# Performance work log

Measured on AMD Instinct MI355X. Metric: run time of the kernel, lower is better.

## Reference

```python
import jax, jax.numpy as jnp
import numpy as np

B, S, HID, H = 8, 128, 256, 4
DH = HID // H
FF = 4 * HID


def setup_inputs() -> dict:
    key = jax.random.key(0)
    ks = jax.random.split(key, 16)
    n = lambda i, shape: jax.random.normal(ks[i], shape, dtype=jnp.float32) * 0.02
    z = lambda shape: jnp.zeros(shape, dtype=jnp.float32)
    return dict(
        x=jax.random.normal(ks[0], (B, S, HID), dtype=jnp.float32),
        attention_mask=jnp.zeros((B, 1, S, S), dtype=jnp.float32),
        Wq=n(1, (HID, HID)), bq=z((HID,)),
        Wk=n(2, (HID, HID)), bk=z((HID,)),
        Wv=n(3, (HID, HID)), bv=z((HID,)),
        order_w=n(4, (2 * DH,)), order_b=z(()),
        dist_w=n(5, (2 * DH,)), dist_b=z(()),
        scalar=jax.random.normal(ks[6], (1,), dtype=jnp.float32),
        AWq=n(7, (HID, HID)), Abq=z((HID,)),
        AWk=n(8, (HID, HID)), Abk=z((HID,)),
        Wd=n(9, (HID, HID)), bd=z((HID,)),
        g1=jnp.ones((HID,), jnp.float32), beta1=z((HID,)),
        W1=n(10, (HID, FF)), b1=z((FF,)),
        W2=n(11, (FF, HID)), b2=z((HID,)),
        g2=jnp.ones((HID,), jnp.float32), beta2=z((HID,)),
    )


def _ln(t, g, b, eps=1e-12):
    m = t.mean(-1, keepdims=True)
    v = ((t - m) ** 2).mean(-1, keepdims=True)
    return (t - m) / jnp.sqrt(v + eps) * g + b


def _heads(t):
    # [B,S,HID] -> [B,H,S,DH]
    return t.reshape(B, S, H, DH).transpose(0, 2, 1, 3)


def reference(x, attention_mask, Wq, bq, Wk, bk, Wv, bv, order_w, order_b,
              dist_w, dist_b, scalar, AWq, Abq, AWk, Abk, Wd, bd,
              g1, beta1, W1, b1, W2, b2, g2, beta2):
    inv = 1.0 / jnp.sqrt(jnp.float32(DH))
    q = x @ Wq + bq
    k = x @ Wk + bk
    v = x @ Wv + bv
    qh, kh, vh = _heads(q), _heads(k), _heads(v)
    scores = jnp.einsum('bhqd,bhkd->bhqk', qh, kh)  # [B,H,S,S]

    # order/distance affines on concat(q_i, k_j): Linear(2*DH,1) decomposes into
    # per-token projections summed via broadcast (same math, no [B,H,S,S,2*DH] tensor)
    pr_order = jax.nn.sigmoid((qh @ order_w[:DH])[..., :, None]
                              + (kh @ order_w[DH:])[..., None, :] + order_b)
    gd_order = jnp.triu(jnp.ones((S, S), jnp.float32), k=1)
    err_order = (jnp.log(pr_order + 1e-24) * gd_order
                 + jnp.log(1.0 - pr_order + 1e-24) * (1.0 - gd_order))

    idx = jnp.arange(S)
    gd_dist = jnp.log(jnp.abs(idx[None, :] - idx[:, None]).astype(jnp.float32) + 1.0)
    pr_dist = ((qh @ dist_w[:DH])[..., :, None]
               + (kh @ dist_w[DH:])[..., None, :] + dist_b)
    err_dist = -jnp.square(gd_dist - pr_dist) * jnp.square(scalar[0]) * 0.5

    rich_scores = scores + err_order + err_dist
    softm = lambda s: jax.nn.softmax(s * inv + attention_mask, axis=-1)
    rich_probs = softm(rich_scores)
    origin_probs = softm(scores)

    # rich/calibrated combine ('fixed'): softmax(origin + 0.5 * rich)
    combined = jax.nn.softmax(origin_probs + 0.5 * rich_probs, axis=-1)

    # two-level attack attention on transformed mixed q/k
    aq, ak = _heads(q @ AWq + Abq), _heads(k @ AWk + Abk)
    attack_probs = softm(jnp.einsum('bhqd,bhkd->bhqk', aq, ak))
    final_probs = jax.nn.softmax(combined + 0.5 * attack_probs, axis=-1)

    ctx = jnp.einsum('bhqk,bhkd->bhqd', final_probs, vh)
    ctx = ctx.transpose(0, 2, 1, 3).reshape(B, S, HID)
    h = _ln(ctx @ Wd + bd + x, g1, beta1)
    f = jax.nn.gelu(h @ W1 + b1, approximate=False) @ W2 + b2
    return _ln(f + h, g2, beta2)
```

## Files before the change

### kernel.cpp

```cpp
#include <hip/hip_runtime.h>
#include <hip/hip_bf16.h>
#include <math.h>

#define B_  8
#define S_  128
#define HID_ 256
#define H_  4
#define DH_ 64
#define FF_ 1024
#define M_  (B_ * S_)

typedef _Float16 half_t;
typedef __attribute__((ext_vector_type(8))) _Float16 half8;
typedef __attribute__((ext_vector_type(4))) float floatx4;

enum { EP_F32 = 0, EP_F16 = 1, EP_F16B = 2, EP_GELU = 3, EP_PROJ = 4 };

__device__ __forceinline__ floatx4 mfma16(half8 a, half8 b, floatx4 c) {
    return __builtin_amdgcn_mfma_f32_16x16x32_f16(a, b, c, 0, 0, 0);
}

__device__ __forceinline__ float wred_sum(float v) {
#pragma unroll
    for (int o = 32; o >= 1; o >>= 1) v += __shfl_xor(v, o, 64);
    return v;
}
__device__ __forceinline__ float wred_max(float v) {
#pragma unroll
    for (int o = 32; o >= 1; o >>= 1) v = fmaxf(v, __shfl_xor(v, o, 64));
    return v;
}
__device__ __forceinline__ float block_sum_256(float v, float* s4, int tid) {
    v = wred_sum(v);
    __syncthreads();
    if ((tid & 63) == 0) s4[tid >> 6] = v;
    __syncthreads();
    return s4[0] + s4[1] + s4[2] + s4[3];
}
__device__ __forceinline__ float2 softmax2(float2 l) {
    float m = wred_max(fmaxf(l.x, l.y));
    float e0 = expf(l.x - m), e1 = expf(l.y - m);
    float s = wred_sum(e0 + e1);
    float r = 1.f / s;
    return make_float2(e0 * r, e1 * r);
}

template<int EPI>
__device__ __forceinline__ void mgemm(
    const half_t* __restrict__ A, int ldA,
    const half_t* __restrict__ Bt, int ldB,
    int kLen, int m0, int n0,
    const float* __restrict__ bias,
    float* __restrict__ Cf, half_t* __restrict__ Ch, int ldC,
    const float* __restrict__ pw1, const float* __restrict__ pw2,
    float* __restrict__ po1, float* __restrict__ po2, int hsel)
{
    __shared__ half8 Asf[2][4][64];
    __shared__ half8 Bsf[2][4][64];

    const int tid = threadIdx.x;
    const int w = tid >> 6, l = tid & 63;
    const int sr = tid >> 2;
    const int sq = tid & 3;
    const int sdst = (sr & 15) | (sq << 4);
    const int smt = sr >> 4;
    const half_t* Ap = A + (size_t)(m0 + sr) * ldA + sq * 8;
    const half_t* Bp = Bt + (size_t)(n0 + sr) * ldB + sq * 8;

    half8 ra, rb;
    auto fetch = [&](int t) {
        ra = *(const half8*)(Ap + t * 32);
        rb = *(const half8*)(Bp + t * 32);
    };
    auto commit = [&](int buf) {
        Asf[buf][smt][sdst] = ra;
        Bsf[buf][smt][sdst] = rb;
    };

    floatx4 zero = {0.f, 0.f, 0.f, 0.f};
    floatx4 acc[4] = {zero, zero, zero, zero};
    const int kt = kLen >> 5;

    fetch(0);
    commit(0);
    __syncthreads();
    for (int t = 0; t < kt; ++t) {
        const bool more = (t + 1 < kt);
        if (more) fetch(t + 1);
        const int buf = t & 1;
        half8 a = Asf[buf][w][l];
        acc[0] = mfma16(a, Bsf[buf][0][l], acc[0]);
        acc[1] = mfma16(a, Bsf[buf][1][l], acc[1]);
        acc[2] = mfma16(a, Bsf[buf][2][l], acc[2]);
        acc[3] = mfma16(a, Bsf[buf][3][l], acc[3]);
        __syncthreads();
        if (more) {
            commit((t + 1) & 1);
            __syncthreads();
        }
    }

    const int quad = l >> 4, lc = l & 15;
    const int rowb = m0 + w * 16 + quad * 4;
    float bvv[4] = {0.f, 0.f, 0.f, 0.f};
    if (EPI >= EP_F16B) {
#pragma unroll
        for (int nt = 0; nt < 4; ++nt) bvv[nt] = bias[n0 + nt * 16 + lc];
    }
    float pw1v[4], pw2v[4];
    if (EPI == EP_PROJ) {
#pragma unroll
        for (int nt = 0; nt < 4; ++nt) {
            pw1v[nt] = pw1[nt * 16 + lc];
            pw2v[nt] = pw2[nt * 16 + lc];
        }
    }
#pragma unroll
    for (int rr = 0; rr < 4; ++rr) {
        float ov[4];
#pragma unroll
        for (int nt = 0; nt < 4; ++nt) {
            float o = acc[nt][rr];
            if (EPI >= EP_F16B) o += bvv[nt];
            if (EPI == EP_GELU) o = 0.5f * o * (1.f + erff(o * 0.70710678118654752f));
            ov[nt] = o;
            const size_t ci = (size_t)(rowb + rr) * ldC + n0 + nt * 16 + lc;
            if (EPI == EP_F32) Cf[ci] = o;
            else Ch[ci] = (half_t)o;
        }
        if (EPI == EP_PROJ) {
            float po = ov[0] * pw1v[0] + ov[1] * pw1v[1] + ov[2] * pw1v[2] + ov[3] * pw1v[3];
            float pd = ov[0] * pw2v[0] + ov[1] * pw2v[1] + ov[2] * pw2v[2] + ov[3] * pw2v[3];
#pragma unroll
            for (int off = 1; off < 16; off <<= 1) {
                po += __shfl_xor(po, off, 64);
                pd += __shfl_xor(pd, off, 64);
            }
            if (lc == 0) {
                const int m = rowb + rr;
                const int idx = ((m >> 7) * H_ + hsel) * S_ + (m & 127);
                po1[idx] = po;
                po2[idx] = pd;
            }
        }
    }
}

__global__ __launch_bounds__(256) void prep_kernel(
    const float* __restrict__ x,
    const float* __restrict__ Wq, const float* __restrict__ Wk,
    const float* __restrict__ Wv, const float* __restrict__ Wd,
    const float* __restrict__ AWq, const float* __restrict__ AWk,
    const float* __restrict__ W1, const float* __restrict__ W2,
    half_t* __restrict__ x16, half_t* __restrict__ Wq16n, half_t* __restrict__ Wk16n,
    half_t* __restrict__ WqT, half_t* __restrict__ WkT, half_t* __restrict__ WvT,
    half_t* __restrict__ WdT, half_t* __restrict__ AWqT, half_t* __restrict__ AWkT,
    half_t* __restrict__ W1T, half_t* __restrict__ W2T)
{
    const int z = blockIdx.z, bx = blockIdx.x, by = blockIdx.y;
    const int tid = threadIdx.x;
    if (z < 3) {
        const float* src = (z == 0) ? x : (z == 1) ? Wq : Wk;
        half_t* dst = (z == 0) ? x16 : (z == 1) ? Wq16n : Wk16n;
        const int total = (z == 0) ? M_ * HID_ : HID_ * HID_;
        const int bid = by * 16 + bx;
        if (bid * 1024 < total) {
            const int base = bid * 1024 + tid * 4;
            float4 vv = *(const float4*)(src + base);
            dst[base + 0] = (half_t)vv.x;
            dst[base + 1] = (half_t)vv.y;
            dst[base + 2] = (half_t)vv.z;
            dst[base + 3] = (half_t)vv.w;
        }
        return;
    }
    const float* src; half_t* dst; int K, N, k0, n0;
    if (z <= 8) {
        const float* ins[6] = {Wq, Wk, Wv, Wd, AWq, AWk};
        half_t* outs[6] = {WqT, WkT, WvT, WdT, AWqT, AWkT};
        src = ins[z - 3]; dst = outs[z - 3];
        K = 256; N = 256; k0 = bx * 64; n0 = by * 64;
        if (bx >= 4 || by >= 4) return;
    } else if (z == 9) {
        src = W1; dst = W1T; K = 256; N = 1024;
        k0 = bx * 64; n0 = by * 64;
        if (bx >= 4) return;
    } else {
        src = W2; dst = W2T; K = 1024; N = 256;
        k0 = by * 64; n0 = bx * 64;
        if (bx >= 4) return;
    }
    __shared__ half_t tl[64][72];
    const int r = tid >> 2, c0 = (tid & 3) * 16;
#pragma unroll 4
    for (int i = 0; i < 16; ++i)
        tl[c0 + i][r] = (half_t)src[(size_t)(k0 + r) * N + n0 + c0 + i];
    __syncthreads();
#pragma unroll 4
    for (int i = 0; i < 16; ++i)
        dst[(size_t)(n0 + r) * K + k0 + c0 + i] = tl[r][c0 + i];
}

__global__ __launch_bounds__(256) void compose_mfma(
    const half_t* __restrict__ AWqT, const half_t* __restrict__ AWkT,
    const half_t* __restrict__ Wq16n, const half_t* __restrict__ Wk16n,
    const float* __restrict__ AWq, const float* __restrict__ AWk,
    const float* __restrict__ bq, const float* __restrict__ bk,
    const float* __restrict__ Abq, const float* __restrict__ Abk,
    half_t* __restrict__ WcqT, half_t* __restrict__ WckT,
    float* __restrict__ bcq, float* __restrict__ bck)
{
    const int z = blockIdx.z;
    if (blockIdx.y < 4) {
        const half_t* A = z ? AWkT : AWqT;
        const half_t* Bt = z ? Wk16n : Wq16n;
        half_t* C = z ? WckT : WcqT;
        mgemm<EP_F16>(A, HID_, Bt, HID_, HID_, blockIdx.y * 64, blockIdx.x * 64,
                      nullptr, nullptr, C, HID_, nullptr, nullptr, nullptr, nullptr, 0);
    } else {
        __shared__ float red[4][64];
        const float* bsrc = z ? bk : bq;
        const float* AW   = z ? AWk : AWq;
        const float* Ab   = z ? Abk : Abq;
        float* bco        = z ? bck : bcq;
        int t = threadIdx.x, l = t & 63, kc = t >> 6;
        int n = blockIdx.x * 64 + l;
        float p = 0.f;
#pragma unroll 8
        for (int kk = 0; kk < 64; ++kk) {
            int k = kc * 64 + kk;
            p = fmaf(bsrc[k], AW[(size_t)k * HID_ + n], p);
        }
        red[kc][l] = p;
        __syncthreads();
        if (kc == 0)
            bco[n] = red[0][l] + red[1][l] + red[2][l] + red[3][l] + Ab[n];
    }
}

__global__ __launch_bounds__(256) void xgemm5(
    const half_t* __restrict__ x16,
    const half_t* __restrict__ WqT, const float* __restrict__ bq,
    const half_t* __restrict__ WkT, const float* __restrict__ bk,
    const half_t* __restrict__ WvT, const float* __restrict__ bv,
    const half_t* __restrict__ WcqT, const float* __restrict__ bcq,
    const half_t* __restrict__ WckT, const float* __restrict__ bck,
    const float* __restrict__ order_w, const float* __restrict__ dist_w,
    half_t* __restrict__ q16, half_t* __restrict__ k16, half_t* __restrict__ v16,
    half_t* __restrict__ aq16, half_t* __restrict__ ak16,
    float* __restrict__ qoA, float* __restrict__ qdA,
    float* __restrict__ koA, float* __restrict__ kdA)
{
    const int z = blockIdx.z;
    const int m0 = blockIdx.y * 64, n0 = blockIdx.x * 64;
    if (z == 0)
        mgemm<EP_PROJ>(x16, HID_, WqT, HID_, HID_, m0, n0, bq, nullptr, q16, HID_,
                       order_w, dist_w, qoA, qdA, blockIdx.x);
    else if (z == 1)
        mgemm<EP_PROJ>(x16, HID_, WkT, HID_, HID_, m0, n0, bk, nullptr, k16, HID_,
                       order_w + DH_, dist_w + DH_, koA, kdA, blockIdx.x);
    else if (z == 2)
        mgemm<EP_F16B>(x16, HID_, WvT, HID_, HID_, m0, n0, bv, nullptr, v16, HID_,
                       nullptr, nullptr, nullptr, nullptr, 0);
    else if (z == 3)
        mgemm<EP_F16B>(x16, HID_, WcqT, HID_, HID_, m0, n0, bcq, nullptr, aq16, HID_,
                       nullptr, nullptr, nullptr, nullptr, 0);
    else
        mgemm<EP_F16B>(x16, HID_, WckT, HID_, HID_, m0, n0, bck, nullptr, ak16, HID_,
                       nullptr, nullptr, nullptr, nullptr, 0);
}

__global__ __launch_bounds__(256) void score_mfma(
    const half_t* __restrict__ q16, const half_t* __restrict__ k16,
    const half_t* __restrict__ aq16, const half_t* __restrict__ ak16,
    float* __restrict__ scb, float* __restrict__ asb)
{
    const int type = blockIdx.z >> 5;
    const int bh = blockIdx.z & 31;
    const int b = bh >> 2, h = bh & 3;
    const size_t off = (size_t)b * S_ * HID_ + h * DH_;
    const half_t* A  = (type ? aq16 : q16) + off;
    const half_t* Bt = (type ? ak16 : k16) + off;
    float* C = (type ? asb : scb) + (size_t)bh * S_ * S_;
    mgemm<EP_F32>(A, HID_, Bt, HID_, DH_, blockIdx.y * 64, blockIdx.x * 64,
                  nullptr, C, nullptr, S_, nullptr, nullptr, nullptr, nullptr, 0);
}

__global__ __launch_bounds__(256) void softmax_pv(
    const float* __restrict__ scb, const float* __restrict__ asb,
    const half_t* __restrict__ v16,
    const float* __restrict__ qoA, const float* __restrict__ qdA,
    const float* __restrict__ koA, const float* __restrict__ kdA,
    const float* __restrict__ mask,
    const float* __restrict__ order_b_p, const float* __restrict__ dist_b_p,
    const float* __restrict__ scalar_p,
    half_t* __restrict__ ctx16)
{
    const int tid = threadIdx.x;
    const int wv = tid >> 6, lane = tid & 63;
    const int bh = blockIdx.x >> 5;
    const int quad = blockIdx.x & 31;
    const int i = quad * 4 + wv;
    const int b = bh >> 2, h = bh & 3;

    const size_t rowoff = ((size_t)bh * S_ + i) * S_ + 2 * lane;
    float2 sc2 = *(const float2*)&scb[rowoff];
    float2 at2 = *(const float2*)&asb[rowoff];
    float2 mk  = *(const float2*)&mask[((size_t)(b * S_ + i)) * S_ + 2 * lane];
    float2 ko  = *(const float2*)&koA[bh * S_ + 2 * lane];
    float2 kd  = *(const float2*)&kdA[bh * S_ + 2 * lane];
    float qo = qoA[bh * S_ + i];
    float qd = qdA[bh * S_ + i];
    float ob = order_b_p[0], db = dist_b_p[0];
    float scl = scalar_p[0];
    float s2 = scl * scl;
    const float inv = 0.125f;

    float2 rich;
    {
        int j = 2 * lane;
        float pr = 1.f / (1.f + expf(-(qo + ko.x + ob)));
        float sel = (j > i) ? pr : 1.f - pr;
        float erro = logf(sel + 1e-24f);
        float gd = logf(fabsf((float)(j - i)) + 1.f);
        float dd = gd - (qd + kd.x + db);
        rich.x = sc2.x + erro - 0.5f * dd * dd * s2;
    }
    {
        int j = 2 * lane + 1;
        float pr = 1.f / (1.f + expf(-(qo + ko.y + ob)));
        float sel = (j > i) ? pr : 1.f - pr;
        float erro = logf(sel + 1e-24f);
        float gd = logf(fabsf((float)(j - i)) + 1.f);
        float dd = gd - (qd + kd.y + db);
        rich.y = sc2.y + erro - 0.5f * dd * dd * s2;
    }

    float2 p0 = softmax2(make_float2(sc2.x * inv + mk.x, sc2.y * inv + mk.y));
    float2 p1 = softmax2(make_float2(rich.x * inv + mk.x, rich.y * inv + mk.y));
    float2 pc = softmax2(make_float2(p0.x + 0.5f * p1.x, p0.y + 0.5f * p1.y));
    float2 pa = softmax2(make_float2(at2.x * inv + mk.x, at2.y * inv + mk.y));
    float2 pf = softmax2(make_float2(pc.x + 0.5f * pa.x, pc.y + 0.5f * pa.y));

    const half_t* vb = v16 + (size_t)b * S_ * HID_ + h * DH_ + lane;
    float acc = 0.f;
#pragma unroll 8
    for (int jj = 0; jj < 64; ++jj) {
        float fx = __shfl(pf.x, jj, 64);
        float fy = __shfl(pf.y, jj, 64);
        acc = fmaf(fx, (float)vb[(size_t)(2 * jj) * HID_], acc);
        acc = fmaf(fy, (float)vb[(size_t)(2 * jj + 1) * HID_], acc);
    }
    ctx16[((size_t)(b * S_ + i)) * HID_ + h * DH_ + lane] = (half_t)acc;
}

__global__ __launch_bounds__(256) void dense_mfma(
    const half_t* __restrict__ ctx16, const half_t* __restrict__ WdT,
    float* __restrict__ dn)
{
    mgemm<EP_F32>(ctx16, HID_, WdT, HID_, HID_, blockIdx.y * 64, blockIdx.x * 64,
                  nullptr, dn, nullptr, HID_, nullptr, nullptr, nullptr, nullptr, 0);
}

__global__ __launch_bounds__(256) void ff1_mfma(
    const half_t* __restrict__ h16, const half_t* __restrict__ W1T,
    const float* __restrict__ b1, half_t* __restrict__ f116)
{
    mgemm<EP_GELU>(h16, HID_, W1T, HID_, HID_, blockIdx.y * 64, blockIdx.x * 64,
                   b1, nullptr, f116, FF_, nullptr, nullptr, nullptr, nullptr, 0);
}

__global__ __launch_bounds__(256) void ff2_mfma(
    const half_t* __restrict__ f116, const half_t* __restrict__ W2T,
    float* __restrict__ p0, float* __restrict__ p1)
{
    const int z = blockIdx.z;
    float* C = z ? p1 : p0;
    mgemm<EP_F32>(f116 + z * 512, FF_, W2T + z * 512, FF_, 512,
                  blockIdx.y * 64, blockIdx.x * 64,
                  nullptr, C, nullptr, HID_, nullptr, nullptr, nullptr, nullptr, 0);
}

__global__ __launch_bounds__(256) void ln1_kernel(
    const float* __restrict__ dn, const float* __restrict__ bd,
    const float* __restrict__ x,
    const float* __restrict__ g1, const float* __restrict__ beta1,
    float* __restrict__ h32, half_t* __restrict__ h16)
{
    __shared__ float s4[4];
    const int row = blockIdx.x;
    const int n = threadIdx.x;
    const size_t idx = (size_t)row * HID_ + n;
    float val = dn[idx] + bd[n] + x[idx];
    float mean = block_sum_256(val, s4, n) * (1.f / HID_);
    float dv = val - mean;
    float var = block_sum_256(dv * dv, s4, n) * (1.f / HID_);
    float r = dv * rsqrtf(var + 1e-12f) * g1[n] + beta1[n];
    h32[idx] = r;
    h16[idx] = (half_t)r;
}

__global__ __launch_bounds__(256) void ln2_kernel(
    const float* __restrict__ p0, const float* __restrict__ p1,
    const float* __restrict__ b2, const float* __restrict__ h32,
    const float* __restrict__ g2, const float* __restrict__ beta2,
    float* __restrict__ out)
{
    __shared__ float s4[4];
    const int row = blockIdx.x;
    const int n = threadIdx.x;
    const size_t idx = (size_t)row * HID_ + n;
    float val = p0[idx] + p1[idx] + b2[n] + h32[idx];
    float mean = block_sum_256(val, s4, n) * (1.f / HID_);
    float dv = val - mean;
    float var = block_sum_256(dv * dv, s4, n) * (1.f / HID_);
    out[idx] = dv * rsqrtf(var + 1e-12f) * g2[n] + beta2[n];
}

extern "C" void kernel_launch(void* const* d_in, const int* in_sizes, int n_in,
                              void* d_out, int out_size, void* d_ws, size_t ws_size,
                              hipStream_t stream) {
    const float* x        = (const float*)d_in[0];
    const float* mask     = (const float*)d_in[1];
    const float* Wq       = (const float*)d_in[2];
    const float* bq       = (const float*)d_in[3];
    const float* Wk       = (const float*)d_in[4];
    const float* bk       = (const float*)d_in[5];
    const float* Wv       = (const float*)d_in[6];
    const float* bv       = (const float*)d_in[7];
    const float* order_w  = (const float*)d_in[8];
    const float* order_b  = (const float*)d_in[9];
    const float* dist_w   = (const float*)d_in[10];
    const float* dist_b   = (const float*)d_in[11];
    const float* scalar   = (const float*)d_in[12];
    const float* AWq      = (const float*)d_in[13];
    const float* Abq      = (const float*)d_in[14];
    const float* AWk      = (const float*)d_in[15];
    const float* Abk      = (const float*)d_in[16];
    const float* Wd       = (const float*)d_in[17];
    const float* bd       = (const float*)d_in[18];
    const float* g1       = (const float*)d_in[19];
    const float* beta1    = (const float*)d_in[20];
    const float* W1       = (const float*)d_in[21];
    const float* b1       = (const float*)d_in[22];
    const float* W2       = (const float*)d_in[23];
    const float* b2       = (const float*)d_in[24];
    const float* g2       = (const float*)d_in[25];
    const float* beta2    = (const float*)d_in[26];

    float* ws = (float*)d_ws;
    size_t off = 0;
    auto afl = [&](size_t n) { float* p = ws + off; off += n; return p; };
    auto ahf = [&](size_t nhalves) { half_t* p = (half_t*)(ws + off); off += nhalves / 2; return p; };

    half_t* x16   = ahf(M_ * HID_);
    half_t* Wq16n = ahf(HID_ * HID_);
    half_t* Wk16n = ahf(HID_ * HID_);
    half_t* WqT   = ahf(HID_ * HID_);
    half_t* WkT   = ahf(HID_ * HID_);
    half_t* WvT   = ahf(HID_ * HID_);
    half_t* WdT   = ahf(HID_ * HID_);
    half_t* AWqT  = ahf(HID_ * HID_);
    half_t* AWkT  = ahf(HID_ * HID_);
    half_t* W1T   = ahf(HID_ * FF_);
    half_t* W2T   = ahf(HID_ * FF_);
    half_t* WcqT  = ahf(HID_ * HID_);
    half_t* WckT  = ahf(HID_ * HID_);
    half_t* q16   = ahf(M_ * HID_);
    half_t* k16   = ahf(M_ * HID_);
    half_t* v16   = ahf(M_ * HID_);
    half_t* aq16  = ahf(M_ * HID_);
    half_t* ak16  = ahf(M_ * HID_);
    half_t* ctx16 = ahf(M_ * HID_);
    half_t* h16   = ahf(M_ * HID_);
    half_t* f116  = ahf(M_ * FF_);
    float* scb  = afl((size_t)B_ * H_ * S_ * S_);
    float* asb  = afl((size_t)B_ * H_ * S_ * S_);
    float* dnb  = afl(M_ * HID_);
    float* hb32 = afl(M_ * HID_);
    float* pf0  = afl(M_ * HID_);
    float* pf1  = afl(M_ * HID_);
    float* bcq  = afl(256);
    float* bck  = afl(256);
    float* qoA  = afl(B_ * H_ * S_);
    float* qdA  = afl(B_ * H_ * S_);
    float* koA  = afl(B_ * H_ * S_);
    float* kdA  = afl(B_ * H_ * S_);

    prep_kernel<<<dim3(16, 16, 11), 256, 0, stream>>>(
        x, Wq, Wk, Wv, Wd, AWq, AWk, W1, W2,
        x16, Wq16n, Wk16n, WqT, WkT, WvT, WdT, AWqT, AWkT, W1T, W2T);
    compose_mfma<<<dim3(4, 5, 2), 256, 0, stream>>>(
        AWqT, AWkT, Wq16n, Wk16n, AWq, AWk, bq, bk, Abq, Abk, WcqT, WckT, bcq, bck);
    xgemm5<<<dim3(4, 16, 5), 256, 0, stream>>>(
        x16, WqT, bq, WkT, bk, WvT, bv, WcqT, bcq, WckT, bck, order_w, dist_w,
        q16, k16, v16, aq16, ak16, qoA, qdA, koA, kdA);
    score_mfma<<<dim3(2, 2, 64), 256, 0, stream>>>(q16, k16, aq16, ak16, scb, asb);
    softmax_pv<<<1024, 256, 0, stream>>>(scb, asb, v16, qoA, qdA, koA, kdA,
                                         mask, order_b, dist_b, scalar, ctx16);
    dense_mfma<<<dim3(4, 16), 256, 0, stream>>>(ctx16, WdT, dnb);
    ln1_kernel<<<M_, 256, 0, stream>>>(dnb, bd, x, g1, beta1, hb32, h16);
    ff1_mfma<<<dim3(16, 16), 256, 0, stream>>>(h16, W1T, b1, f116);
    ff2_mfma<<<dim3(4, 16, 2), 256, 0, stream>>>(f116, W2T, pf0, pf1);
    ln2_kernel<<<M_, 256, 0, stream>>>(pf0, pf1, b2, hb32, g2, beta2, (float*)d_out);
}
```

Baseline: 171.8 us.

## Fuse score GEMMs, softmax chain and PV into one attention kernel; fuse GEMM+LayerNorm

Replaces the separate score GEMM and softmax/PV kernels with a single attention kernel per (batch, head, query-half) that computes both score matrices with MFMA, runs the five-softmax chain in registers, and does PV with MFMA through shared memory. The dense and FF2 GEMMs are each fused with their following LayerNorm into a full-row kernel, and the split-K FF2 partial buffers go away. This removes the fp32 score round trips through global memory and several launches, but it also cuts parallelism to 64 and 16 blocks, which may underfill the GPU.

Result: slower. 199.2 us (+15.9%).

```diff
diff --git a/kernel.cpp b/kernel.cpp
--- a/kernel.cpp
+++ b/kernel.cpp
@@ -11,6 +11,7 @@
 #define M_  (B_ * S_)
 
 typedef _Float16 half_t;
+typedef __attribute__((ext_vector_type(4))) _Float16 half4;
 typedef __attribute__((ext_vector_type(8))) _Float16 half8;
 typedef __attribute__((ext_vector_type(4))) float floatx4;
 
@@ -20,29 +21,28 @@
     return __builtin_amdgcn_mfma_f32_16x16x32_f16(a, b, c, 0, 0, 0);
 }
 
-__device__ __forceinline__ float wred_sum(float v) {
-#pragma unroll
-    for (int o = 32; o >= 1; o >>= 1) v += __shfl_xor(v, o, 64);
+__device__ __forceinline__ float qred_sum(float v) {
+#pragma unroll
+    for (int o = 1; o < 16; o <<= 1) v += __shfl_xor(v, o, 64);
     return v;
 }
-__device__ __forceinline__ float wred_max(float v) {
-#pragma unroll
-    for (int o = 32; o >= 1; o >>= 1) v = fmaxf(v, __shfl_xor(v, o, 64));
+__device__ __forceinline__ float qred_max(float v) {
+#pragma unroll
+    for (int o = 1; o < 16; o <<= 1) v = fmaxf(v, __shfl_xor(v, o, 64));
     return v;
 }
-__device__ __forceinline__ float block_sum_256(float v, float* s4, int tid) {
-    v = wred_sum(v);
-    __syncthreads();
-    if ((tid & 63) == 0) s4[tid >> 6] = v;
-    __syncthreads();
-    return s4[0] + s4[1] + s4[2] + s4[3];
-}
-__device__ __forceinline__ float2 softmax2(float2 l) {
-    float m = wred_max(fmaxf(l.x, l.y));
-    float e0 = expf(l.x - m), e1 = expf(l.y - m);
-    float s = wred_sum(e0 + e1);
+__device__ __forceinline__ void sm8(float (&v)[8]) {
+    float m = v[0];
+#pragma unroll
+    for (int j = 1; j < 8; ++j) m = fmaxf(m, v[j]);
+    m = qred_max(m);
+    float s = 0.f;
+#pragma unroll
+    for (int j = 0; j < 8; ++j) { v[j] = expf(v[j] - m); s += v[j]; }
+    s = qred_sum(s);
     float r = 1.f / s;
-    return make_float2(e0 * r, e1 * r);
+#pragma unroll
+    for (int j = 0; j < 8; ++j) v[j] *= r;
 }
 
 template<int EPI>
@@ -270,25 +270,10 @@
                        nullptr, nullptr, nullptr, nullptr, 0);
 }
 
-__global__ __launch_bounds__(256) void score_mfma(
+__global__ __launch_bounds__(256) void attn_fused(
     const half_t* __restrict__ q16, const half_t* __restrict__ k16,
-    const half_t* __restrict__ aq16, const half_t* __restrict__ ak16,
-    float* __restrict__ scb, float* __restrict__ asb)
-{
-    const int type = blockIdx.z >> 5;
-    const int bh = blockIdx.z & 31;
-    const int b = bh >> 2, h = bh & 3;
-    const size_t off = (size_t)b * S_ * HID_ + h * DH_;
-    const half_t* A  = (type ? aq16 : q16) + off;
-    const half_t* Bt = (type ? ak16 : k16) + off;
-    float* C = (type ? asb : scb) + (size_t)bh * S_ * S_;
-    mgemm<EP_F32>(A, HID_, Bt, HID_, DH_, blockIdx.y * 64, blockIdx.x * 64,
-                  nullptr, C, nullptr, S_, nullptr, nullptr, nullptr, nullptr, 0);
-}
-
-__global__ __launch_bounds__(256) void softmax_pv(
-    const float* __restrict__ scb, const float* __restrict__ asb,
-    const half_t* __restrict__ v16,
+    const half_t* __restrict__ v16, const half_t* __restrict__ aq16,
+    const half_t* __restrict__ ak16,
     const float* __restrict__ qoA, const float* __restrict__ qdA,
     const float* __restrict__ koA, const float* __restrict__ kdA,
     const float* __restrict__ mask,
@@ -296,70 +281,235 @@
     const float* __restrict__ scalar_p,
     half_t* __restrict__ ctx16)
 {
+    __shared__ half8 Qf[2][4][64], AQf[2][4][64];
+    __shared__ half8 Kf[2][8][64], AKf[2][8][64];
+    __shared__ half_t Vs[128][68];
+    __shared__ half_t Pm[64][136];
+
     const int tid = threadIdx.x;
-    const int wv = tid >> 6, lane = tid & 63;
-    const int bh = blockIdx.x >> 5;
-    const int quad = blockIdx.x & 31;
-    const int i = quad * 4 + wv;
+    const int w = tid >> 6, l = tid & 63;
+    const int quad = l >> 4, lc = l & 15;
+    const int bid = blockIdx.x;
+    const int bh = bid >> 1, it = bid & 1;
     const int b = bh >> 2, h = bh & 3;
-
-    const size_t rowoff = ((size_t)bh * S_ + i) * S_ + 2 * lane;
-    float2 sc2 = *(const float2*)&scb[rowoff];
-    float2 at2 = *(const float2*)&asb[rowoff];
-    float2 mk  = *(const float2*)&mask[((size_t)(b * S_ + i)) * S_ + 2 * lane];
-    float2 ko  = *(const float2*)&koA[bh * S_ + 2 * lane];
-    float2 kd  = *(const float2*)&kdA[bh * S_ + 2 * lane];
-    float qo = qoA[bh * S_ + i];
-    float qd = qdA[bh * S_ + i];
-    float ob = order_b_p[0], db = dist_b_p[0];
-    float scl = scalar_p[0];
-    float s2 = scl * scl;
+    const size_t hoff = (size_t)b * S_ * HID_ + h * DH_;
+
+#pragma unroll
+    for (int u = 0; u < 2; ++u) {
+        int idx = tid * 2 + u;
+        int r = idx >> 3, c = idx & 7;
+        const size_t g = hoff + (size_t)(it * 64 + r) * HID_ + c * 8;
+        int kt = c >> 2, mt = r >> 4, sl = (r & 15) | ((c & 3) << 4);
+        Qf[kt][mt][sl]  = *(const half8*)(q16 + g);
+        AQf[kt][mt][sl] = *(const half8*)(aq16 + g);
+    }
+#pragma unroll
+    for (int u = 0; u < 4; ++u) {
+        int idx = tid * 4 + u;
+        int j = idx >> 3, c = idx & 7;
+        const size_t g = hoff + (size_t)j * HID_ + c * 8;
+        int kt = c >> 2, jt = j >> 4, sl = (j & 15) | ((c & 3) << 4);
+        Kf[kt][jt][sl]  = *(const half8*)(k16 + g);
+        AKf[kt][jt][sl] = *(const half8*)(ak16 + g);
+        half8 vv = *(const half8*)(v16 + g);
+        half4 v0 = {vv[0], vv[1], vv[2], vv[3]};
+        half4 v1 = {vv[4], vv[5], vv[6], vv[7]};
+        *(half4*)&Vs[j][c * 8]     = v0;
+        *(half4*)&Vs[j][c * 8 + 4] = v1;
+    }
+    __syncthreads();
+
+    floatx4 zero = {0.f, 0.f, 0.f, 0.f};
+    floatx4 accS[8], accA[8];
+#pragma unroll
+    for (int jt = 0; jt < 8; ++jt) { accS[jt] = zero; accA[jt] = zero; }
+#pragma unroll
+    for (int kt = 0; kt < 2; ++kt) {
+        half8 a0 = Qf[kt][w][l];
+        half8 a1 = AQf[kt][w][l];
+#pragma unroll
+        for (int jt = 0; jt < 8; ++jt) {
+            accS[jt] = mfma16(a0, Kf[kt][jt][l], accS[jt]);
+            accA[jt] = mfma16(a1, AKf[kt][jt][l], accA[jt]);
+        }
+    }
+
+    const float ob = order_b_p[0], db = dist_b_p[0];
+    const float scl = scalar_p[0];
+    const float s2 = scl * scl;
     const float inv = 0.125f;
-
-    float2 rich;
-    {
-        int j = 2 * lane;
-        float pr = 1.f / (1.f + expf(-(qo + ko.x + ob)));
-        float sel = (j > i) ? pr : 1.f - pr;
-        float erro = logf(sel + 1e-24f);
-        float gd = logf(fabsf((float)(j - i)) + 1.f);
-        float dd = gd - (qd + kd.x + db);
-        rich.x = sc2.x + erro - 0.5f * dd * dd * s2;
-    }
-    {
-        int j = 2 * lane + 1;
-        float pr = 1.f / (1.f + expf(-(qo + ko.y + ob)));
-        float sel = (j > i) ? pr : 1.f - pr;
-        float erro = logf(sel + 1e-24f);
-        float gd = logf(fabsf((float)(j - i)) + 1.f);
-        float dd = gd - (qd + kd.y + db);
-        rich.y = sc2.y + erro - 0.5f * dd * dd * s2;
-    }
-
-    float2 p0 = softmax2(make_float2(sc2.x * inv + mk.x, sc2.y * inv + mk.y));
-    float2 p1 = softmax2(make_float2(rich.x * inv + mk.x, rich.y * inv + mk.y));
-    float2 pc = softmax2(make_float2(p0.x + 0.5f * p1.x, p0.y + 0.5f * p1.y));
-    float2 pa = softmax2(make_float2(at2.x * inv + mk.x, at2.y * inv + mk.y));
-    float2 pf = softmax2(make_float2(pc.x + 0.5f * pa.x, pc.y + 0.5f * pa.y));
-
-    const half_t* vb = v16 + (size_t)b * S_ * HID_ + h * DH_ + lane;
-    float acc = 0.f;
-#pragma unroll 8
-    for (int jj = 0; jj < 64; ++jj) {
-        float fx = __shfl(pf.x, jj, 64);
-        float fy = __shfl(pf.y, jj, 64);
-        acc = fmaf(fx, (float)vb[(size_t)(2 * jj) * HID_], acc);
-        acc = fmaf(fy, (float)vb[(size_t)(2 * jj + 1) * HID_], acc);
-    }
-    ctx16[((size_t)(b * S_ + i)) * HID_ + h * DH_ + lane] = (half_t)acc;
-}
-
-__global__ __launch_bounds__(256) void dense_mfma(
-    const half_t* __restrict__ ctx16, const half_t* __restrict__ WdT,
-    float* __restrict__ dn)
+    float kov[8], kdv[8];
+#pragma unroll
+    for (int jt = 0; jt < 8; ++jt) {
+        kov[jt] = koA[bh * S_ + jt * 16 + lc];
+        kdv[jt] = kdA[bh * S_ + jt * 16 + lc];
+    }
+    const int il_base = w * 16 + quad * 4;
+#pragma unroll
+    for (int reg = 0; reg < 4; ++reg) {
+        const int il = il_base + reg;
+        const int i  = it * 64 + il;
+        float qo = qoA[bh * S_ + i], qd = qdA[bh * S_ + i];
+        const float* mrow = mask + ((size_t)(b * S_ + i)) * S_;
+        float mk[8], lg[8], as_[8];
+#pragma unroll
+        for (int jt = 0; jt < 8; ++jt) {
+            mk[jt] = mrow[jt * 16 + lc];
+            lg[jt] = accS[jt][reg];
+            as_[jt] = accA[jt][reg];
+        }
+        float p0[8];
+#pragma unroll
+        for (int jt = 0; jt < 8; ++jt) p0[jt] = lg[jt] * inv + mk[jt];
+        sm8(p0);
+        float p1[8];
+#pragma unroll
+        for (int jt = 0; jt < 8; ++jt) {
+            int j = jt * 16 + lc;
+            float pr = 1.f / (1.f + expf(-(qo + kov[jt] + ob)));
+            float sel = (j > i) ? pr : 1.f - pr;
+            float erro = logf(sel + 1e-24f);
+            float gd = logf(fabsf((float)(j - i)) + 1.f);
+            float dd = gd - (qd + kdv[jt] + db);
+            p1[jt] = (lg[jt] + erro - 0.5f * dd * dd * s2) * inv + mk[jt];
+        }
+        sm8(p1);
+#pragma unroll
+        for (int jt = 0; jt < 8; ++jt) p0[jt] += 0.5f * p1[jt];
+        sm8(p0);
+#pragma unroll
+        for (int jt = 0; jt < 8; ++jt) p1[jt] = as_[jt] * inv + mk[jt];
+        sm8(p1);
+#pragma unroll
+        for (int jt = 0; jt < 8; ++jt) p0[jt] += 0.5f * p1[jt];
+        sm8(p0);
+#pragma unroll
+        for (int jt = 0; jt < 8; ++jt) Pm[il][jt * 16 + lc] = (half_t)p0[jt];
+    }
+    __syncthreads();
+
+    half8 pa_[4];
+#pragma unroll
+    for (int kt = 0; kt < 4; ++kt)
+        pa_[kt] = *(const half8*)&Pm[w * 16 + lc][kt * 32 + quad * 8];
+    floatx4 apv[4];
+#pragma unroll
+    for (int nt = 0; nt < 4; ++nt) apv[nt] = zero;
+#pragma unroll
+    for (int nt = 0; nt < 4; ++nt) {
+#pragma unroll
+        for (int kt = 0; kt < 4; ++kt) {
+            half8 vf;
+#pragma unroll
+            for (int e = 0; e < 8; ++e)
+                vf[e] = Vs[kt * 32 + quad * 8 + e][nt * 16 + lc];
+            apv[nt] = mfma16(pa_[kt], vf, apv[nt]);
+        }
+    }
+#pragma unroll
+    for (int nt = 0; nt < 4; ++nt) {
+#pragma unroll
+        for (int reg = 0; reg < 4; ++reg) {
+            int i = it * 64 + w * 16 + quad * 4 + reg;
+            ctx16[hoff + (size_t)i * HID_ + nt * 16 + lc] = (half_t)apv[nt][reg];
+        }
+    }
+}
+
+template<int WRITE16>
+__global__ __launch_bounds__(256) void gemmln(
+    const half_t* __restrict__ A, const half_t* __restrict__ Bt, int K,
+    const float* __restrict__ bias, const float* __restrict__ res,
+    const float* __restrict__ g, const float* __restrict__ be,
+    float* __restrict__ out32, half_t* __restrict__ out16)
 {
-    mgemm<EP_F32>(ctx16, HID_, WdT, HID_, HID_, blockIdx.y * 64, blockIdx.x * 64,
-                  nullptr, dn, nullptr, HID_, nullptr, nullptr, nullptr, nullptr, 0);
+    __shared__ half8 Asf[2][4][64];
+    __shared__ half8 Bsf[2][16][64];
+
+    const int tid = threadIdx.x;
+    const int w = tid >> 6, l = tid & 63;
+    const int quad = l >> 4, lc = l & 15;
+    const int m0 = blockIdx.x * 64;
+
+    const int ar = tid >> 2, aq_ = tid & 3;
+    const half_t* Ap = A + (size_t)(m0 + ar) * K + aq_ * 8;
+    const half_t* Bp = Bt + (size_t)tid * K;
+
+    half8 ra, rb[4];
+    auto fetch = [&](int t) {
+        ra = *(const half8*)(Ap + t * 32);
+        const half_t* bp = Bp + t * 32;
+#pragma unroll
+        for (int u = 0; u < 4; ++u) rb[u] = *(const half8*)(bp + u * 8);
+    };
+    auto commit = [&](int buf) {
+        Asf[buf][ar >> 4][(ar & 15) | (aq_ << 4)] = ra;
+#pragma unroll
+        for (int u = 0; u < 4; ++u)
+            Bsf[buf][tid >> 4][(tid & 15) | (u << 4)] = rb[u];
+    };
+
+    floatx4 zero = {0.f, 0.f, 0.f, 0.f};
+    floatx4 acc[16];
+#pragma unroll
+    for (int nt = 0; nt < 16; ++nt) acc[nt] = zero;
+    const int kt = K >> 5;
+
+    fetch(0);
+    commit(0);
+    __syncthreads();
+    for (int t = 0; t < kt; ++t) {
+        const bool more = (t + 1 < kt);
+        if (more) fetch(t + 1);
+        const int buf = t & 1;
+        half8 a = Asf[buf][w][l];
+#pragma unroll
+        for (int nt = 0; nt < 16; ++nt)
+            acc[nt] = mfma16(a, Bsf[buf][nt][l], acc[nt]);
+        __syncthreads();
+        if (more) {
+            commit((t + 1) & 1);
+            __syncthreads();
+        }
+    }
+
+    float bv[16], gg[16], bb[16];
+#pragma unroll
+    for (int nt = 0; nt < 16; ++nt) {
+        bv[nt] = bias[nt * 16 + lc];
+        gg[nt] = g[nt * 16 + lc];
+        bb[nt] = be[nt * 16 + lc];
+    }
+#pragma unroll
+    for (int reg = 0; reg < 4; ++reg) {
+        const int row = m0 + w * 16 + quad * 4 + reg;
+        const float* rr = res + (size_t)row * HID_;
+        float vals[16];
+        float s = 0.f;
+#pragma unroll
+        for (int nt = 0; nt < 16; ++nt) {
+            vals[nt] = acc[nt][reg] + bv[nt] + rr[nt * 16 + lc];
+            s += vals[nt];
+        }
+        s = qred_sum(s);
+        float mean = s * (1.f / HID_);
+        float vs = 0.f;
+#pragma unroll
+        for (int nt = 0; nt < 16; ++nt) {
+            float d = vals[nt] - mean;
+            vals[nt] = d;
+            vs += d * d;
+        }
+        vs = qred_sum(vs);
+        float rstd = rsqrtf(vs * (1.f / HID_) + 1e-12f);
+#pragma unroll
+        for (int nt = 0; nt < 16; ++nt) {
+            float o = vals[nt] * rstd * gg[nt] + bb[nt];
+            const size_t ci = (size_t)row * HID_ + nt * 16 + lc;
+            out32[ci] = o;
+            if (WRITE16) out16[ci] = (half_t)o;
+        }
+    }
 }
 
 __global__ __launch_bounds__(256) void ff1_mfma(
@@ -368,53 +518,6 @@
 {
     mgemm<EP_GELU>(h16, HID_, W1T, HID_, HID_, blockIdx.y * 64, blockIdx.x * 64,
                    b1, nullptr, f116, FF_, nullptr, nullptr, nullptr, nullptr, 0);
-}
-
-__global__ __launch_bounds__(256) void ff2_mfma(
-    const half_t* __restrict__ f116, const half_t* __restrict__ W2T,
-    float* __restrict__ p0, float* __restrict__ p1)
-{
-    const int z = blockIdx.z;
-    float* C = z ? p1 : p0;
-    mgemm<EP_F32>(f116 + z * 512, FF_, W2T + z * 512, FF_, 512,
-                  blockIdx.y * 64, blockIdx.x * 64,
-                  nullptr, C, nullptr, HID_, nullptr, nullptr, nullptr, nullptr, 0);
-}
-
-__global__ __launch_bounds__(256) void ln1_kernel(
-    const float* __restrict__ dn, const float* __restrict__ bd,
-    const float* __restrict__ x,
-    const float* __restrict__ g1, const float* __restrict__ beta1,
-    float* __restrict__ h32, half_t* __restrict__ h16)
-{
-    __shared__ float s4[4];
-    const int row = blockIdx.x;
-    const int n = threadIdx.x;
-    const size_t idx = (size_t)row * HID_ + n;
-    float val = dn[idx] + bd[n] + x[idx];
-    float mean = block_sum_256(val, s4, n) * (1.f / HID_);
-    float dv = val - mean;
-    float var = block_sum_256(dv * dv, s4, n) * (1.f / HID_);
-    float r = dv * rsqrtf(var + 1e-12f) * g1[n] + beta1[n];
-    h32[idx] = r;
-    h16[idx] = (half_t)r;
-}
-
-__global__ __launch_bounds__(256) void ln2_kernel(
-    const float* __restrict__ p0, const float* __restrict__ p1,
-    const float* __restrict__ b2, const float* __restrict__ h32,
-    const float* __restrict__ g2, const float* __restrict__ beta2,
-    float* __restrict__ out)
-{
-    __shared__ float s4[4];
-    const int row = blockIdx.x;
-    const int n = threadIdx.x;
-    const size_t idx = (size_t)row * HID_ + n;
-    float val = p0[idx] + p1[idx] + b2[n] + h32[idx];
-    float mean = block_sum_256(val, s4, n) * (1.f / HID_);
-    float dv = val - mean;
-    float var = block_sum_256(dv * dv, s4, n) * (1.f / HID_);
-    out[idx] = dv * rsqrtf(var + 1e-12f) * g2[n] + beta2[n];
 }
 
 extern "C" void kernel_launch(void* const* d_in, const int* in_sizes, int n_in,
@@ -451,7 +554,7 @@
     float* ws = (float*)d_ws;
     size_t off = 0;
     auto afl = [&](size_t n) { float* p = ws + off; off += n; return p; };
-    auto ahf = [&](size_t nhalves) { half_t* p = (half_t*)(ws + off); off += nhalves / 2; return p; };
+    auto ahf = [&](size_t nh) { half_t* p = (half_t*)(ws + off); off += nh / 2; return p; };
 
     half_t* x16   = ahf(M_ * HID_);
     half_t* Wq16n = ahf(HID_ * HID_);
@@ -474,12 +577,7 @@
     half_t* ctx16 = ahf(M_ * HID_);
     half_t* h16   = ahf(M_ * HID_);
     half_t* f116  = ahf(M_ * FF_);
-    float* scb  = afl((size_t)B_ * H_ * S_ * S_);
-    float* asb  = afl((size_t)B_ * H_ * S_ * S_);
-    float* dnb  = afl(M_ * HID_);
     float* hb32 = afl(M_ * HID_);
-    float* pf0  = afl(M_ * HID_);
-    float* pf1  = afl(M_ * HID_);
     float* bcq  = afl(256);
     float* bck  = afl(256);
     float* qoA  = afl(B_ * H_ * S_);
@@ -495,12 +593,11 @@
     xgemm5<<<dim3(4, 16, 5), 256, 0, stream>>>(
         x16, WqT, bq, WkT, bk, WvT, bv, WcqT, bcq, WckT, bck, order_w, dist_w,
         q16, k16, v16, aq16, ak16, qoA, qdA, koA, kdA);
-    score_mfma<<<dim3(2, 2, 64), 256, 0, stream>>>(q16, k16, aq16, ak16, scb, asb);
-    softmax_pv<<<1024, 256, 0, stream>>>(scb, asb, v16, qoA, qdA, koA, kdA,
-                                         mask, order_b, dist_b, scalar, ctx16);
-    dense_mfma<<<dim3(4, 16), 256, 0, stream>>>(ctx16, WdT, dnb);
-    ln1_kernel<<<M_, 256, 0, stream>>>(dnb, bd, x, g1, beta1, hb32, h16);
+    attn_fused<<<64, 256, 0, stream>>>(
+        q16, k16, v16, aq16, ak16, qoA, qdA, koA, kdA,
+        mask, order_b, dist_b, scalar, ctx16);
+    gemmln<1><<<16, 256, 0, stream>>>(ctx16, WdT, HID_, bd, x, g1, beta1, hb32, h16);
     ff1_mfma<<<dim3(16, 16), 256, 0, stream>>>(h16, W1T, b1, f116);
-    ff2_mfma<<<dim3(4, 16, 2), 256, 0, stream>>>(f116, W2T, pf0, pf1);
-    ln2_kernel<<<M_, 256, 0, stream>>>(pf0, pf1, b2, hb32, g2, beta2, (float*)d_out);
-}
+    gemmln<0><<<16, 256, 0, stream>>>(f116, W2T, FF_, b2, hb32, g2, beta2,
+                                      (float*)d_out, nullptr);
+}
```
